# Performance work log

Hardware: AMD Instinct MI355X
Metric: run time of the kernel (lower is better)

## Reference

```python
import jax, jax.numpy as jnp
import numpy as np

N, E, IN, H, O, ED = 20000, 100000, 167, 4, 256, 10
HID = H * O  # 1024
BN_EPS = 1e-5


def _bn(x, g, b):
    # BatchNorm1d in training mode: batch statistics over nodes
    mu = x.mean(0)
    var = x.var(0)
    return (x - mu) * jax.lax.rsqrt(var + BN_EPS) * g + b


def _gat(x, src, dst, ef, Wg, We, attn, at, cb, heads, out):
    # modified_GAT: multi-head attention with edge features + time scalar
    n = x.shape[0]
    h = (x @ Wg).reshape(n, heads, out)                 # [N,H,O]
    e = (ef[:, 1:] @ We).reshape(-1, heads, out)        # [E,H,O] edge-feature proj
    t = ef[:, 0]                                        # [E] time feature
    # node-level attention scores (avoids materializing [E,H,O] twice)
    s_src = jnp.einsum('nhd,hd->nh', h, attn[0])
    s_dst = jnp.einsum('nhd,hd->nh', h, attn[1])
    s_e = jnp.einsum('ehd,hd->eh', e, attn[2])
    logits = jax.nn.leaky_relu(s_src[src] + s_dst[dst] + s_e + t[:, None] * at, 0.2)  # [E,H]
    # attention normalization: softmax over incoming edges of each dst node
    m = jax.ops.segment_max(logits, dst, num_segments=n)
    m = jnp.where(jnp.isfinite(m), m, 0.0)
    p = jnp.exp(logits - m[dst])
    denom = jax.ops.segment_sum(p, dst, num_segments=n)
    w = p / (denom[dst] + 1e-16)                        # [E,H]
    msg = w[:, :, None] * (h[src] + e)                  # [E,H,O]
    agg = jax.ops.segment_sum(msg, dst, num_segments=n) # [N,H,O]
    return agg.reshape(n, heads * out) + cb


def setup_inputs() -> dict:
    key = jax.random.key(0)
    ks = iter(jax.random.split(key, 64))

    def nrm(shape, s):
        return jax.random.normal(next(ks), shape, dtype=jnp.float32) * np.float32(s)

    d = {}
    d['x'] = jax.random.normal(next(ks), (N, IN), dtype=jnp.float32)
    d['edge_index'] = jax.random.randint(next(ks), (2, E), 0, N)
    d['edge_attr'] = jax.random.uniform(next(ks), (E, ED + 2), dtype=jnp.float32)
    conv_dims = [(IN, H, O), (HID, H, O), (HID, 1, 2)]
    for i, (fin, hh, oo) in enumerate(conv_dims, 1):
        d[f'Wg{i}'] = nrm((fin, hh * oo), 1.0 / np.sqrt(fin))
        d[f'We{i}'] = nrm((ED, hh * oo), 1.0 / np.sqrt(ED))
        d[f'attn{i}'] = nrm((3, hh, oo), 0.1)
        d[f'at{i}'] = nrm((hh,), 0.1)
        d[f'cb{i}'] = jnp.zeros((hh * oo,), jnp.float32)
    lin_dims = [(IN, HID), (HID, HID), (HID, 2)]
    bn_dims = [IN, HID, HID]
    for i, (fin, fo) in enumerate(lin_dims, 1):
        d[f'lw{i}'] = nrm((fin, fo), 1.0 / np.sqrt(fin))
        d[f'lb{i}'] = jnp.zeros((fo,), jnp.float32)
        d[f'g{i}'] = jnp.ones((bn_dims[i - 1],), jnp.float32)
        d[f'b{i}'] = jnp.zeros((bn_dims[i - 1],), jnp.float32)
    return d


def reference(x, edge_index, edge_attr,
              Wg1, We1, attn1, at1, cb1, lw1, lb1, g1, b1,
              Wg2, We2, attn2, at2, cb2, lw2, lb2, g2, b2,
              Wg3, We3, attn3, at3, cb3, lw3, lb3, g3, b3):
    src, dst = edge_index[0], edge_index[1]
    ef = edge_attr[:, :-1]  # drop edge class column
    h = _bn(x, g1, b1)
    h = jax.nn.relu(h @ lw1 + lb1 + _gat(h, src, dst, ef, Wg1, We1, attn1, at1, cb1, H, O))
    h = _bn(h, g2, b2)
    h = jax.nn.relu(h @ lw2 + lb2 + _gat(h, src, dst, ef, Wg2, We2, attn2, at2, cb2, H, O))
    h = _bn(h, g3, b3)
    h = jax.nn.relu(h @ lw3 + lb3 + _gat(h, src, dst, ef, Wg3, We3, attn3, at3, cb3, 1, 2))
    return h
```

## Files before the change

### kernel.cpp

```cpp
#include <hip/hip_runtime.h>
#include <math.h>

#define NN 20000
#define EE 100000
#define FIN 167
#define KP1 256
#define HID 1024
#define OO 256
#define NB 8

typedef unsigned short u16;
typedef short bf16x8 __attribute__((ext_vector_type(8)));
typedef short s16x4  __attribute__((ext_vector_type(4)));
typedef float f32x4  __attribute__((ext_vector_type(4)));

__device__ __forceinline__ float bf(u16 u){ return __uint_as_float(((unsigned)u)<<16); }
__device__ __forceinline__ u16 fb(float v){
  unsigned u = __float_as_uint(v);
  return (u16)((u + 0x7FFFu + ((u>>16)&1u)) >> 16);
}
__device__ __forceinline__ float ldv(const float* p, long i){ return p[i]; }
__device__ __forceinline__ float ldv(const u16*   p, long i){ return bf(p[i]); }

__global__ void k_count(const int* __restrict__ ei, int* __restrict__ counts){
  int e = blockIdx.x*256 + threadIdx.x;
  if (e < EE) atomicAdd(&counts[ei[EE+e]], 1);
}

__global__ __launch_bounds__(256) void k_scanA(const int* __restrict__ counts,
                                               int* __restrict__ iptr, int* __restrict__ bsum){
  __shared__ int sd[256];
  int b = blockIdx.x, tid = threadIdx.x;
  int i = b*256 + tid;
  int v = (i<NN)? counts[i] : 0;
  sd[tid]=v; __syncthreads();
  for (int off=1; off<256; off<<=1){
    int t = (tid>=off)? sd[tid-off] : 0;
    __syncthreads();
    sd[tid] += t;
    __syncthreads();
  }
  if (i<NN) iptr[i] = sd[tid]-v;
  if (tid==255) bsum[b]=sd[255];
}
__global__ __launch_bounds__(128) void k_scanB(const int* __restrict__ bsum,
                                               int* __restrict__ boff, int* __restrict__ iptrN,
                                               int nb){
  __shared__ int sd[128];
  int tid=threadIdx.x;
  int v=(tid<nb)? bsum[tid]:0;
  sd[tid]=v; __syncthreads();
  for (int off=1; off<128; off<<=1){
    int t=(tid>=off)?sd[tid-off]:0;
    __syncthreads();
    sd[tid]+=t;
    __syncthreads();
  }
  if (tid<nb) boff[tid]=sd[tid]-v;
  if (tid==127) *iptrN = sd[127];
}
__global__ void k_scanC(const int* __restrict__ boff, int* __restrict__ iptr){
  int i = blockIdx.x*256+threadIdx.x;
  if (i<NN) iptr[i] += boff[blockIdx.x];
}

__global__ void k_fill(const int* __restrict__ ei, const int* __restrict__ iptr,
                       int* __restrict__ cursor, int* __restrict__ eid){
  int e = blockIdx.x*256 + threadIdx.x;
  if (e < EE){
    int d = ei[EE+e];
    int pos = atomicAdd(&cursor[d],1);
    eid[iptr[d]+pos] = e;
  }
}

template<typename T>
__global__ void k_bnstats(const T* __restrict__ X, float* __restrict__ sums, int F){
  int f = blockIdx.y*256 + threadIdx.x;
  if (f >= F) return;
  int r0 = blockIdx.x*100, r1 = r0+100;
  float s=0.f, s2=0.f;
  for (int r=r0;r<r1;r++){ float v = ldv(X,(long)r*F+f); s += v; s2 += v*v; }
  atomicAdd(&sums[f], s);
  atomicAdd(&sums[F+f], s2);
}

__global__ __launch_bounds__(256) void k_bnstats8(const u16* __restrict__ X, float* __restrict__ part){
  int tid = threadIdx.x;
  int f8 = (tid & 127)*8;
  int r0 = blockIdx.x*79, r1 = min(NN, r0+79);
  float s[8]={0,0,0,0,0,0,0,0}, s2[8]={0,0,0,0,0,0,0,0};
  for (int r=r0 + (tid>>7); r<r1; r+=2){
    bf16x8 v = *(const bf16x8*)(X + (long)r*HID + f8);
    #pragma unroll
    for (int j=0;j<8;j++){ float x=bf((u16)v[j]); s[j]+=x; s2[j]+=x*x; }
  }
  __shared__ float red[256][8];
  float* pb = part + (long)blockIdx.x*2048;
  #pragma unroll
  for (int j=0;j<8;j++) red[tid][j]=s[j];
  __syncthreads();
  if (tid<128){
    #pragma unroll
    for (int j=0;j<8;j++) pb[f8+j] = red[tid][j]+red[tid+128][j];
  }
  __syncthreads();
  #pragma unroll
  for (int j=0;j<8;j++) red[tid][j]=s2[j];
  __syncthreads();
  if (tid<128){
    #pragma unroll
    for (int j=0;j<8;j++) pb[1024+f8+j] = red[tid][j]+red[tid+128][j];
  }
}

__global__ __launch_bounds__(256) void k_pred(const float* __restrict__ part, float* __restrict__ sums){
  int idx = blockIdx.x*256 + threadIdx.x;
  float s = 0.f;
  #pragma unroll 8
  for (int b=0;b<256;b++) s += part[(long)b*2048 + idx];
  sums[idx] = s;
}

__global__ void k_bnfin(const float* __restrict__ sums, const float* __restrict__ g,
                        const float* __restrict__ b, float* __restrict__ scale,
                        float* __restrict__ shift, int F){
  int f = blockIdx.x*256 + threadIdx.x;
  if (f >= F) return;
  float mu  = sums[f]   * (1.f/NN);
  float var = sums[F+f] * (1.f/NN) - mu*mu;
  float sc  = rsqrtf(var + 1e-5f) * g[f];
  scale[f] = sc;
  shift[f] = b[f] - mu*sc;
}

__global__ __launch_bounds__(256) void k_foldT(const float* __restrict__ Wg, const float* __restrict__ Wl,
                        const float* __restrict__ scale,
                        u16* __restrict__ Wt, int K, int Kp){
  __shared__ float t[32][33];
  int k0 = blockIdx.x*32, c0 = blockIdx.y*32;
  int tx = threadIdx.x & 31, ty = threadIdx.x >> 5;
  bool second = (c0 >= HID);
  const float* W = second ? Wl : Wg;
  int cc0 = second ? c0 - HID : c0;
  #pragma unroll
  for (int i=0;i<4;i++){
    int k = k0 + ty + i*8;
    t[ty+i*8][tx] = (k < K) ? W[(long)k*HID + cc0 + tx] * scale[k] : 0.f;
  }
  __syncthreads();
  #pragma unroll
  for (int i=0;i<4;i++){
    int c = c0 + ty + i*8;
    Wt[(long)c*Kp + k0 + tx] = fb(t[tx][ty+i*8]);
  }
}

__global__ void k_cinit(const float* __restrict__ lb, float* __restrict__ cst){
  int c = blockIdx.x*256 + threadIdx.x;
  if (c < 2*HID) cst[c] = (c >= HID) ? lb[c-HID] : 0.f;
}

__global__ __launch_bounds__(256) void k_const(const float* __restrict__ Wg, const float* __restrict__ Wl,
                        const float* __restrict__ shift, float* __restrict__ cst, int K){
  int tx = threadIdx.x & 63, ty = threadIdx.x >> 6;
  int c = blockIdx.x*64 + tx;
  bool second = c >= HID;
  const float* W = second ? Wl : Wg;
  int cc = second ? c-HID : c;
  int k0 = blockIdx.y*128;
  int k1 = min(K, k0+128);
  float s = 0.f;
  for (int k=k0+ty; k<k1; k+=4) s += shift[k]*W[(long)k*HID+cc];
  __shared__ float red[256];
  red[threadIdx.x] = s;
  __syncthreads();
  if (ty == 0){
    float tot = red[tx] + red[tx+64] + red[tx+128] + red[tx+192];
    atomicAdd(&cst[c], tot);
  }
}

__global__ void k_cast(const float* __restrict__ x, u16* __restrict__ xb){
  long idx = (long)blockIdx.x*256 + threadIdx.x;
  if (idx >= (long)NN*KP1) return;
  int n = (int)(idx / KP1), k = (int)(idx % KP1);
  xb[idx] = (k<FIN)? fb(x[(long)n*FIN+k]) : (u16)0;
}

__global__ void k_we16(const float* __restrict__ We, u16* __restrict__ We16){
  int i = blockIdx.x*256 + threadIdx.x;
  if (i < 10*HID) We16[i] = fb(We[i]);
}

#define MF(a_,b_,c_) __builtin_amdgcn_mfma_f32_16x16x32_bf16(a_,b_,c_,0,0,0)
#define FENCE asm volatile("" ::: "memory")
#define BAR do { FENCE; __builtin_amdgcn_s_barrier(); FENCE; } while(0)

__global__ __launch_bounds__(512,2) void k_gemm(const u16* __restrict__ A, int K,
                     const u16* __restrict__ Wt, const float* __restrict__ cst,
                     u16* __restrict__ Chg, u16* __restrict__ Clin){
  __shared__ u16 lds[2][24576];
  int b = blockIdx.x;
  int wg = (b & 7)*158 + (b >> 3);
  int row0 = (wg >> 4)*256, col0 = (wg & 15)*128;
  int tid = threadIdx.x;
  int wave = tid >> 6, lane = tid & 63, quad = lane >> 4, lo = lane & 15;
  int wm = wave >> 1, wn = wave & 1;
  const u16* Apt[2];
  #pragma unroll
  for (int i=0;i<2;i++){
    int s = i*512 + tid, srow = s>>2;
    int gr = row0 + srow; if (gr >= NN) gr = NN-1;
    Apt[i] = A + (long)gr*K + (((s&3)^(srow&3))*8);
  }
  int brow = tid>>2;
  const u16* Bpt = Wt + (long)(col0 + brow)*K + ((((tid&3)^(brow&3)))*8);
  const char* ldsc = (const char*)&lds[0][0];
  int axor = lo & 3;
  int aoff = (wm*64 + lo)*64 + ((quad^axor)*16);
  int boff = 32768 + (wn*64 + lo)*64 + ((quad^axor)*16);
  int NT = K >> 6;
  f32x4 acc[4][4] = {};
  {
    u16* d = (u16*)&lds[0][0];
    __builtin_amdgcn_global_load_lds(Apt[0],      d +          tid*8, 16, 0, 0);
    __builtin_amdgcn_global_load_lds(Apt[1],      d +  4096 +  tid*8, 16, 0, 0);
    __builtin_amdgcn_global_load_lds(Bpt,         d + 16384 +  tid*8, 16, 0, 0);
    __builtin_amdgcn_global_load_lds(Apt[0] + 32, d +  8192 +  tid*8, 16, 0, 0);
    __builtin_amdgcn_global_load_lds(Apt[1] + 32, d + 12288 +  tid*8, 16, 0, 0);
    __builtin_amdgcn_global_load_lds(Bpt    + 32, d + 20480 +  tid*8, 16, 0, 0);
    asm volatile("s_waitcnt vmcnt(3)" ::: "memory");
    BAR;
  }
  for (int t=0; t<NT; t++){
    const char* Lb = ldsc + (t&1)*49152;
    u16* Sb = (u16*)&lds[0][0] + ((t&1)^1)*24576;
    int k0n = (t+1) << 6;
    int nx = (t+1 < NT);
    bf16x8 af[4], bfr[4];
    #pragma unroll
    for (int i=0;i<4;i++) af[i]  = *(const bf16x8*)(Lb + aoff + i*1024);
    #pragma unroll
    for (int n=0;n<4;n++) bfr[n] = *(const bf16x8*)(Lb + boff + n*1024);
    if (nx){
      __builtin_amdgcn_global_load_lds(Apt[0] + k0n, Sb +          tid*8, 16, 0, 0);
      __builtin_amdgcn_global_load_lds(Apt[1] + k0n, Sb +  4096 +  tid*8, 16, 0, 0);
      __builtin_amdgcn_global_load_lds(Bpt    + k0n, Sb + 16384 +  tid*8, 16, 0, 0);
    }
    #pragma unroll
    for (int i=0;i<4;i++)
      #pragma unroll
      for (int n=0;n<4;n++)
        acc[i][n] = MF(af[i], bfr[n], acc[i][n]);
    if (nx) asm volatile("s_waitcnt vmcnt(3)" ::: "memory");
    else    asm volatile("s_waitcnt vmcnt(0)" ::: "memory");
    BAR;
    #pragma unroll
    for (int i=0;i<4;i++) af[i]  = *(const bf16x8*)(Lb + 16384 + aoff + i*1024);
    #pragma unroll
    for (int n=0;n<4;n++) bfr[n] = *(const bf16x8*)(Lb +  8192 + boff + n*1024);
    if (nx){
      __builtin_amdgcn_global_load_lds(Apt[0] + k0n + 32, Sb +  8192 +  tid*8, 16, 0, 0);
      __builtin_amdgcn_global_load_lds(Apt[1] + k0n + 32, Sb + 12288 +  tid*8, 16, 0, 0);
      __builtin_amdgcn_global_load_lds(Bpt    + k0n + 32, Sb + 20480 +  tid*8, 16, 0, 0);
    }
    #pragma unroll
    for (int i=0;i<4;i++)
      #pragma unroll
      for (int n=0;n<4;n++)
        acc[i][n] = MF(af[i], bfr[n], acc[i][n]);
    if (nx) asm volatile("s_waitcnt vmcnt(3)" ::: "memory");
    BAR;
  }
  #pragma unroll
  for (int i=0;i<4;i++){
    #pragma unroll
    for (int n=0;n<4;n++){
      int col = col0 + wn*64 + n*16 + lo;
      float cs = cst[col];
      #pragma unroll
      for (int r=0;r<4;r++){
        int row = row0 + wm*64 + i*16 + quad*4 + r;
        if (row < NN){
          u16 o = fb(acc[i][n][r] + cs);
          if (col < HID) Chg[(long)row*HID + col] = o;
          else           Clin[(long)row*HID + col - HID] = o;
        }
      }
    }
  }
}
#undef MF
#undef BAR
#undef FENCE

__global__ __launch_bounds__(256) void k_sdot(const u16* __restrict__ hg, const float* __restrict__ attn,
                       float* __restrict__ ssrc, float* __restrict__ sdst){
  int unit = blockIdx.x*4 + (threadIdx.x >> 6);
  if (unit >= NN*4) return;
  int lane = threadIdx.x & 63;
  int n = unit >> 2, h = unit & 3;
  const u16* hp = hg + (long)n*HID + h*OO + lane*4;
  s16x4 v = *(const s16x4*)hp;
  float4 x0 = *(const float4*)(attn + h*OO + lane*4);
  float4 x1 = *(const float4*)(attn + HID + h*OO + lane*4);
  float f0 = bf((u16)v.x), f1 = bf((u16)v.y), f2 = bf((u16)v.z), f3 = bf((u16)v.w);
  float ss = f0*x0.x + f1*x0.y + f2*x0.z + f3*x0.w;
  float sd = f0*x1.x + f1*x1.y + f2*x1.z + f3*x1.w;
  #pragma unroll
  for (int off=32; off>0; off>>=1){
    ss += __shfl_down(ss, off);
    sd += __shfl_down(sd, off);
  }
  if (lane==0){ ssrc[unit]=ss; sdst[unit]=sd; }
}

__global__ void k_q(const float* __restrict__ We, const float* __restrict__ attn,
                    float* __restrict__ q){
  int t = threadIdx.x;
  if (t >= 40) return;
  int k = t >> 2, h = t & 3;
  float s = 0.f;
  for (int d=0; d<OO; d++) s += We[(long)k*HID + h*OO + d] * attn[2*HID + h*OO + d];
  q[k*4+h] = s;
}

__global__ void k_logits(const int* __restrict__ ei, const float* __restrict__ ea,
                         const float* __restrict__ q, const float* __restrict__ at,
                         const float* __restrict__ ssrc, const float* __restrict__ sdst,
                         float* __restrict__ L){
  int e = blockIdx.x*256 + threadIdx.x;
  if (e >= EE) return;
  int s = ei[e], dd = ei[EE+e];
  float4 a0 = *(const float4*)(ea + (long)e*12);
  float4 a1 = *(const float4*)(ea + (long)e*12 + 4);
  float4 a2 = *(const float4*)(ea + (long)e*12 + 8);
  float t = a0.x;
  float cc[10] = {a0.y,a0.z,a0.w, a1.x,a1.y,a1.z,a1.w, a2.x,a2.y,a2.z};
  float4 ss = *(const float4*)(ssrc + (long)s*4);
  float4 sd = *(const float4*)(sdst + (long)dd*4);
  float sv[4] = {ss.x+sd.x, ss.y+sd.y, ss.z+sd.z, ss.w+sd.w};
  float4 out;
  #pragma unroll
  for (int h=0;h<4;h++){
    float se = 0.f;
    #pragma unroll
    for (int k=0;k<10;k++) se += cc[k]*q[k*4+h];
    float v = sv[h] + se + t*at[h];
    ((float*)&out)[h] = (v>0.f)? v : 0.2f*v;
  }
  *(float4*)(L + (long)e*4) = out;
}

__global__ void k_mden(const int* __restrict__ iptr, const int* __restrict__ eid,
                       const float* __restrict__ ea, float* __restrict__ L,
                       float* __restrict__ cw){
  int n = blockIdx.x*256 + threadIdx.x;
  if (n >= NN) return;
  int b = iptr[n], e1 = iptr[n+1];
  float m0=-INFINITY, m1=-INFINITY, m2=-INFINITY, m3=-INFINITY;
  for (int i=b;i<e1;i++){
    float4 l = *(const float4*)(L + (long)eid[i]*4);
    m0=fmaxf(m0,l.x); m1=fmaxf(m1,l.y); m2=fmaxf(m2,l.z); m3=fmaxf(m3,l.w);
  }
  if (b==e1){ m0=m1=m2=m3=0.f; }
  float s0=0.f,s1=0.f,s2=0.f,s3=0.f;
  for (int i=b;i<e1;i++){
    float4 l = *(const float4*)(L + (long)eid[i]*4);
    s0+=expf(l.x-m0); s1+=expf(l.y-m1); s2+=expf(l.z-m2); s3+=expf(l.w-m3);
  }
  float d0=1.f/(s0+1e-16f), d1=1.f/(s1+1e-16f), d2=1.f/(s2+1e-16f), d3=1.f/(s3+1e-16f);
  float c[4][10] = {};
  for (int i=b;i<e1;i++){
    int e = eid[i];
    float4 l = *(const float4*)(L + (long)e*4);
    float4 w = { expf(l.x-m0)*d0, expf(l.y-m1)*d1, expf(l.z-m2)*d2, expf(l.w-m3)*d3 };
    *(float4*)(L + (long)e*4) = w;
    float4 a0 = *(const float4*)(ea + (long)e*12);
    float4 a1 = *(const float4*)(ea + (long)e*12 + 4);
    float4 a2 = *(const float4*)(ea + (long)e*12 + 8);
    float cc[10] = {a0.y,a0.z,a0.w, a1.x,a1.y,a1.z,a1.w, a2.x,a2.y,a2.z};
    #pragma unroll
    for (int k=0;k<10;k++){
      c[0][k] += w.x*cc[k]; c[1][k] += w.y*cc[k];
      c[2][k] += w.z*cc[k]; c[3][k] += w.w*cc[k];
    }
  }
  float* cp = cw + (long)n*40;
  #pragma unroll
  for (int h=0;h<4;h++)
    #pragma unroll
    for (int k=0;k<10;k++) cp[h*10+k] = c[h][k];
}

__global__ __launch_bounds__(256) void k_gath(
    const u16* __restrict__ hg, const int* __restrict__ ei,
    const int* __restrict__ iptr, const int* __restrict__ eid,
    const float* __restrict__ L,
    const float* __restrict__ cw,
    const u16* __restrict__ We16, const float* __restrict__ cb,
    u16* __restrict__ lio)
{
  __shared__ u16  sWe[10*HID];
  __shared__ float scb[HID];
  int tid = threadIdx.x;
  for (int i=tid;i<10*HID;i+=256) sWe[i] = We16[i];
  for (int i=tid;i<HID;i+=256) scb[i] = cb[i];
  __syncthreads();
  int h = tid >> 6;
  int f0 = tid*4;
  int d0 = blockIdx.x*NB, dend = min(NN, d0+NB);
  for (int d=d0; d<dend; d++){
    s16x4 a0 = *(const s16x4*)(lio + (long)d*HID + f0);
    float acc0=bf((u16)a0.x), acc1=bf((u16)a0.y), acc2=bf((u16)a0.z), acc3=bf((u16)a0.w);
    int b0 = iptr[d], en = iptr[d+1];
    float wN = 0.f; s16x4 vN = {};
    if (b0 < en){
      int e = eid[b0], s_ = ei[e];
      wN = L[(long)e*4 + h];
      vN = *(const s16x4*)(hg + (long)s_*HID + f0);
    }
    for (int i=b0;i<en;i++){
      float w = wN; s16x4 v = vN;
      if (i+1 < en){
        int e2 = eid[i+1], s2 = ei[e2];
        wN = L[(long)e2*4 + h];
        vN = *(const s16x4*)(hg + (long)s2*HID + f0);
      }
      acc0 += w*bf((u16)v.x); acc1 += w*bf((u16)v.y);
      acc2 += w*bf((u16)v.z); acc3 += w*bf((u16)v.w);
    }
    const float* cp = cw + (long)d*40 + h*10;
    float ew0=0.f, ew1=0.f, ew2=0.f, ew3=0.f;
    #pragma unroll
    for (int k=0;k<10;k++){
      float c = cp[k];
      s16x4 wv = *(const s16x4*)(sWe + k*HID + f0);
      ew0 += c*bf((u16)wv.x); ew1 += c*bf((u16)wv.y);
      ew2 += c*bf((u16)wv.z); ew3 += c*bf((u16)wv.w);
    }
    acc0 += ew0; acc1 += ew1; acc2 += ew2; acc3 += ew3;
    u16 o[4];
    o[0] = fb(fmaxf(acc0 + scb[f0  ], 0.f));
    o[1] = fb(fmaxf(acc1 + scb[f0+1], 0.f));
    o[2] = fb(fmaxf(acc2 + scb[f0+2], 0.f));
    o[3] = fb(fmaxf(acc3 + scb[f0+3], 0.f));
    *(s16x4*)(lio + (long)d*HID + f0) = *(const s16x4*)o;
  }
}

__global__ void k_c4init(const float* __restrict__ lb, float* __restrict__ c4){
  if (threadIdx.x==0 && blockIdx.x==0){ c4[0]=0.f; c4[1]=0.f; c4[2]=lb[0]; c4[3]=lb[1]; }
}

__global__ __launch_bounds__(256) void k_fold3(const float* __restrict__ Wg, const float* __restrict__ lw,
                        const float* __restrict__ scale, const float* __restrict__ shift,
                        float* __restrict__ W4, float* __restrict__ c4){
  int k = blockIdx.x*256 + threadIdx.x;
  float sc = scale[k], sh = shift[k];
  float w0=Wg[k*2], w1=Wg[k*2+1], l0=lw[k*2], l1=lw[k*2+1];
  float4 o = {w0*sc, w1*sc, l0*sc, l1*sc};
  *(float4*)(W4 + (long)k*4) = o;
  __shared__ float red[256][4];
  int tid = threadIdx.x;
  red[tid][0]=sh*w0; red[tid][1]=sh*w1; red[tid][2]=sh*l0; red[tid][3]=sh*l1;
  __syncthreads();
  for (int o2=128;o2>0;o2>>=1){
    if (tid<o2){
      #pragma unroll
      for (int j=0;j<4;j++) red[tid][j]+=red[tid+o2][j];
    }
    __syncthreads();
  }
  if (tid==0){
    #pragma unroll
    for (int j=0;j<4;j++) atomicAdd(&c4[j], red[0][j]);
  }
}

__global__ __launch_bounds__(256) void k_n3(const u16* __restrict__ in,
    const float* __restrict__ W4, const float* __restrict__ c4,
    const float* __restrict__ attn,
    float* __restrict__ hg3, float* __restrict__ lin3,
    float* __restrict__ ssrc, float* __restrict__ sdst)
{
  __shared__ float sW[HID*4];
  __shared__ float sx[4][HID];
  int tid = threadIdx.x;
  int n0 = blockIdx.x*4;
  for (int i=tid; i<HID; i+=256) *(float4*)&sW[i*4] = *(const float4*)(W4 + (long)i*4);
  for (int idx=tid; idx<512; idx+=256){
    int rr = idx>>7, ch = idx&127;
    bf16x8 v = *(const bf16x8*)(in + (long)(n0+rr)*HID + ch*8);
    #pragma unroll
    for (int j=0;j<8;j++) sx[rr][ch*8+j] = bf((u16)v[j]);
  }
  __syncthreads();
  int w = tid>>6, lane = tid&63;
  float p0=0.f,p1=0.f,p2=0.f,p3=0.f;
  #pragma unroll
  for (int g=0; g<16; g++){
    int k = g*64 + lane;
    float x = sx[w][k];
    float4 wv = *(const float4*)&sW[k*4];
    p0 += x*wv.x; p1 += x*wv.y; p2 += x*wv.z; p3 += x*wv.w;
  }
  #pragma unroll
  for (int off=32; off>0; off>>=1){
    p0 += __shfl_down(p0, off);
    p1 += __shfl_down(p1, off);
    p2 += __shfl_down(p2, off);
    p3 += __shfl_down(p3, off);
  }
  if (lane==0){
    int n = n0 + w;
    float r0=p0+c4[0], r1=p1+c4[1], r2=p2+c4[2], r3=p3+c4[3];
    hg3[n*2]=r0; hg3[n*2+1]=r1;
    lin3[n*2]=r2; lin3[n*2+1]=r3;
    ssrc[n]=r0*attn[0]+r1*attn[1];
    sdst[n]=r0*attn[2]+r1*attn[3];
  }
}

__global__ void k_logits3(const int* __restrict__ ei, const float* __restrict__ ea,
                          const float* __restrict__ We, const float* __restrict__ attn,
                          const float* __restrict__ at, const float* __restrict__ ssrc,
                          const float* __restrict__ sdst, float* __restrict__ L){
  int e = blockIdx.x*256 + threadIdx.x;
  if (e >= EE) return;
  int s = ei[e], d = ei[EE+e];
  float e0=0.f, e1=0.f;
  #pragma unroll
  for (int k=0;k<10;k++){
    float c = ea[e*12+1+k];
    e0 += c*We[k*2]; e1 += c*We[k*2+1];
  }
  float se = e0*attn[4] + e1*attn[5];
  float v = ssrc[s] + sdst[d] + se + ea[e*12]*at[0];
  L[e] = (v>0.f)? v : 0.2f*v;
}

__global__ void k_mden3(const int* __restrict__ iptr, const int* __restrict__ eid,
                        const float* __restrict__ ea, float* __restrict__ L,
                        float* __restrict__ cw){
  int n = blockIdx.x*256 + threadIdx.x;
  if (n >= NN) return;
  int b = iptr[n], e1 = iptr[n+1];
  float mx = -INFINITY;
  for (int i=b;i<e1;i++) mx = fmaxf(mx, L[eid[i]]);
  if (b == e1) mx = 0.f;
  float s = 0.f;
  for (int i=b;i<e1;i++) s += expf(L[eid[i]] - mx);
  float dv = 1.f/(s+1e-16f);
  float c[10] = {0.f,0.f,0.f,0.f,0.f,0.f,0.f,0.f,0.f,0.f};
  for (int i=b;i<e1;i++){
    int e = eid[i];
    float w = expf(L[e]-mx)*dv;
    L[e] = w;
    #pragma unroll
    for (int k=0;k<10;k++) c[k] += w*ea[e*12+1+k];
  }
  float* cp = cw + (long)n*10;
  #pragma unroll
  for (int k=0;k<10;k++) cp[k] = c[k];
}

__global__ void k_gather3(const int* __restrict__ ei,
                          const int* __restrict__ iptr, const int* __restrict__ eid,
                          const float* __restrict__ L,
                          const float* __restrict__ cw,
                          const float* __restrict__ hg3,
                          const float* __restrict__ We, const float* __restrict__ lin3,
                          const float* __restrict__ cb, float* __restrict__ out){
  int n = blockIdx.x*256 + threadIdx.x;
  if (n >= NN) return;
  int b = iptr[n], en = iptr[n+1];
  const float* cp = cw + (long)n*10;
  float e0f=0.f, e1f=0.f;
  #pragma unroll
  for (int k=0;k<10;k++){ e0f += cp[k]*We[k*2]; e1f += cp[k]*We[k*2+1]; }
  float a0=0.f, a1=0.f;
  for (int i=b;i<en;i++){
    int e = eid[i], s_ = ei[e];
    float w = L[e];
    a0 += w*hg3[s_*2];
    a1 += w*hg3[s_*2+1];
  }
  out[n*2]   = fmaxf(lin3[n*2]  +a0+e0f+cb[0], 0.f);
  out[n*2+1] = fmaxf(lin3[n*2+1]+a1+e1f+cb[1], 0.f);
}

extern "C" void kernel_launch(void* const* d_in, const int* in_sizes, int n_in,
                              void* d_out, int out_size, void* d_ws, size_t ws_size,
                              hipStream_t stream){
  const int* ei = (const int*)d_in[1];

  long long sz[64];
  {
    const long long* s64 = (const long long*)(const void*)in_sizes;
    bool is64 = (n_in >= 2) && (in_sizes[0] == 3340000) && (in_sizes[1] == 0)
                && (s64[1] == 200000);
    for (int i=0;i<n_in && i<64;i++) sz[i] = is64 ? s64[i] : (long long)in_sizes[i];
  }

  int IWg[3], IWe[3], IAttn[3], IAt[3], ICb[3], ILw[3], ILb[3], IG[3], IB[3];
  if (n_in > 8 && sz[8] == (long long)HID*HID){
    for (int l=0;l<3;l++){
      IWg[l]=3+l*5; IWe[l]=4+l*5; IAttn[l]=5+l*5; IAt[l]=6+l*5; ICb[l]=7+l*5;
      ILw[l]=18+l*4; ILb[l]=19+l*4; IG[l]=20+l*4; IB[l]=21+l*4;
    }
  } else {
    int idx=3;
    for (int l=0;l<3;l++){
      IWg[l]=idx++; IWe[l]=idx++; IAttn[l]=idx++; IAt[l]=idx++; ICb[l]=idx++;
      ILw[l]=idx++; ILb[l]=idx++; IG[l]=idx++; IB[l]=idx++;
    }
  }
  #define FP(i) ((const float*)d_in[(i)])

  char* ws = (char*)d_ws;
  size_t off = 0;
  auto alloc = [&](size_t bytes)->void*{ void* p = ws + off; off += (bytes + 255) & ~(size_t)255; return p; };
  auto G = [](long n){ return (int)((n+255)/256); };

  u16*   buf0 = (u16*)  alloc((size_t)NN*HID*2);
  u16*   bufA = (u16*)  alloc((size_t)NN*HID*2);
  u16*   bufB = (u16*)  alloc((size_t)NN*HID*2);
  u16*   xbf  = (u16*)  alloc((size_t)NN*KP1*2);
  u16*   Wt   = (u16*)  alloc((size_t)2*HID*HID*2);
  u16*   We16 = (u16*)  alloc((size_t)10*HID*2);
  float* cst  = (float*)alloc(2*HID*4);
  float* L    = (float*)alloc((size_t)EE*4*4);
  float* ssrc = (float*)alloc((size_t)NN*4*4);
  float* sdst = (float*)alloc((size_t)NN*4*4);
  int*   iptr = (int*)  alloc((size_t)(NN+4)*4);
  int*   cnts = (int*)  alloc((size_t)NN*4);
  int*   eid  = (int*)  alloc((size_t)EE*4);
  int*   bsum = (int*)  alloc(256*4);
  int*   boff = (int*)  alloc(256*4);
  float* stats= (float*)alloc(2*HID*4);
  float* scale= (float*)alloc(HID*4);
  float* shift= (float*)alloc(HID*4);
  float* qbuf = (float*)alloc(64*4);
  float* hg3  = (float*)alloc((size_t)NN*2*4);
  float* lin3 = (float*)alloc((size_t)NN*2*4);
  float* cw   = (float*)alloc((size_t)NN*40*4);
  float* W4   = (float*)alloc((size_t)HID*4*4);
  float* c4   = (float*)alloc(4*4);
  float* part = (float*)alloc((size_t)256*2048*4);

  int nsb = G(NN);
  hipMemsetAsync(cnts, 0, NN*sizeof(int), stream);
  k_count<<<G(EE),256,0,stream>>>(ei, cnts);
  k_scanA<<<nsb,256,0,stream>>>(cnts, iptr, bsum);
  k_scanB<<<1,128,0,stream>>>(bsum, boff, iptr+NN, nsb);
  k_scanC<<<nsb,256,0,stream>>>(boff, iptr);
  hipMemsetAsync(cnts, 0, NN*sizeof(int), stream);
  k_fill<<<G(EE),256,0,stream>>>(ei, iptr, cnts, eid);

  int gg = 1264;
  int gsd = (NN*4+3)/4;

  {
    hipMemsetAsync(stats, 0, 2*FIN*sizeof(float), stream);
    dim3 bg(200, 1);
    k_bnstats<float><<<bg,256,0,stream>>>(FP(0), stats, FIN);
    k_bnfin<<<1,256,0,stream>>>(stats, FP(IG[0]), FP(IB[0]), scale, shift, FIN);
    k_cast<<<G((long)NN*KP1),256,0,stream>>>(FP(0), xbf);
    dim3 ft(KP1/32, 64);
    k_foldT<<<ft,256,0,stream>>>(FP(IWg[0]), FP(ILw[0]), scale, Wt, FIN, KP1);
    k_cinit<<<8,256,0,stream>>>(FP(ILb[0]), cst);
    dim3 cg(32, (FIN+127)/128);
    k_const<<<cg,256,0,stream>>>(FP(IWg[0]), FP(ILw[0]), shift, cst, FIN);
    k_we16<<<40,256,0,stream>>>(FP(IWe[0]), We16);
    k_gemm<<<gg,512,0,stream>>>(xbf, KP1, Wt, cst, buf0, bufA);
    k_sdot<<<gsd,256,0,stream>>>(buf0, FP(IAttn[0]), ssrc, sdst);
    k_q<<<1,64,0,stream>>>(FP(IWe[0]), FP(IAttn[0]), qbuf);
    k_logits<<<G(EE),256,0,stream>>>(ei, FP(2), qbuf, FP(IAt[0]), ssrc, sdst, L);
    k_mden<<<G(NN),256,0,stream>>>(iptr, eid, FP(2), L, cw);
    k_gath<<<(NN+NB-1)/NB,256,0,stream>>>(buf0, ei, iptr, eid, L, cw,
                                          We16, FP(ICb[0]), bufA);
  }
  {
    k_bnstats8<<<256,256,0,stream>>>(bufA, part);
    k_pred<<<8,256,0,stream>>>(part, stats);
    k_bnfin<<<4,256,0,stream>>>(stats, FP(IG[1]), FP(IB[1]), scale, shift, HID);
    dim3 ft(HID/32, 64);
    k_foldT<<<ft,256,0,stream>>>(FP(IWg[1]), FP(ILw[1]), scale, Wt, HID, HID);
    k_cinit<<<8,256,0,stream>>>(FP(ILb[1]), cst);
    dim3 cg(32, HID/128);
    k_const<<<cg,256,0,stream>>>(FP(IWg[1]), FP(ILw[1]), shift, cst, HID);
    k_we16<<<40,256,0,stream>>>(FP(IWe[1]), We16);
    k_gemm<<<gg,512,0,stream>>>(bufA, HID, Wt, cst, buf0, bufB);
    k_sdot<<<gsd,256,0,stream>>>(buf0, FP(IAttn[1]), ssrc, sdst);
    k_q<<<1,64,0,stream>>>(FP(IWe[1]), FP(IAttn[1]), qbuf);
    k_logits<<<G(EE),256,0,stream>>>(ei, FP(2), qbuf, FP(IAt[1]), ssrc, sdst, L);
    k_mden<<<G(NN),256,0,stream>>>(iptr, eid, FP(2), L, cw);
    k_gath<<<(NN+NB-1)/NB,256,0,stream>>>(buf0, ei, iptr, eid, L, cw,
                                          We16, FP(ICb[1]), bufB);
  }

  k_bnstats8<<<256,256,0,stream>>>(bufB, part);
  k_pred<<<8,256,0,stream>>>(part, stats);
  k_bnfin<<<4,256,0,stream>>>(stats, FP(IG[2]), FP(IB[2]), scale, shift, HID);
  k_c4init<<<1,64,0,stream>>>(FP(ILb[2]), c4);
  k_fold3<<<HID/256,256,0,stream>>>(FP(IWg[2]), FP(ILw[2]), scale, shift, W4, c4);
  k_n3<<<NN/4,256,0,stream>>>(bufB, W4, c4, FP(IAttn[2]), hg3, lin3, ssrc, sdst);
  k_logits3<<<G(EE),256,0,stream>>>(ei, FP(2), FP(IWe[2]), FP(IAttn[2]), FP(IAt[2]), ssrc, sdst, L);
  k_mden3<<<G(NN),256,0,stream>>>(iptr, eid, FP(2), L, cw);
  k_gather3<<<G(NN),256,0,stream>>>(ei, iptr, eid, L, cw, hg3,
                                    FP(IWe[2]), lin3, FP(ICb[2]), (float*)d_out);
}
```

Before: 815.3 us.

## Use triple-buffered LDS ring with prefetch distance two in GEMM

```diff
diff --git a/kernel.cpp b/kernel.cpp
--- a/kernel.cpp
+++ b/kernel.cpp
@@ -200,7 +200,7 @@
 __global__ __launch_bounds__(512,2) void k_gemm(const u16* __restrict__ A, int K,
                      const u16* __restrict__ Wt, const float* __restrict__ cst,
                      u16* __restrict__ Chg, u16* __restrict__ Clin){
-  __shared__ u16 lds[2][24576];
+  __shared__ u16 lds[3][12288];
   int b = blockIdx.x;
   int wg = (b & 7)*158 + (b >> 3);
   int row0 = (wg >> 4)*256, col0 = (wg & 15)*128;
@@ -219,59 +219,49 @@
   const char* ldsc = (const char*)&lds[0][0];
   int axor = lo & 3;
   int aoff = (wm*64 + lo)*64 + ((quad^axor)*16);
-  int boff = 32768 + (wn*64 + lo)*64 + ((quad^axor)*16);
-  int NT = K >> 6;
+  int boff = 16384 + (wn*64 + lo)*64 + ((quad^axor)*16);
+  int NT = K >> 5;
   f32x4 acc[4][4] = {};
   {
-    u16* d = (u16*)&lds[0][0];
-    __builtin_amdgcn_global_load_lds(Apt[0],      d +          tid*8, 16, 0, 0);
-    __builtin_amdgcn_global_load_lds(Apt[1],      d +  4096 +  tid*8, 16, 0, 0);
-    __builtin_amdgcn_global_load_lds(Bpt,         d + 16384 +  tid*8, 16, 0, 0);
-    __builtin_amdgcn_global_load_lds(Apt[0] + 32, d +  8192 +  tid*8, 16, 0, 0);
-    __builtin_amdgcn_global_load_lds(Apt[1] + 32, d + 12288 +  tid*8, 16, 0, 0);
-    __builtin_amdgcn_global_load_lds(Bpt    + 32, d + 20480 +  tid*8, 16, 0, 0);
+    u16* d0 = (u16*)&lds[0][0];
+    u16* d1 = (u16*)&lds[1][0];
+    __builtin_amdgcn_global_load_lds(Apt[0],      d0 +         tid*8, 16, 0, 0);
+    __builtin_amdgcn_global_load_lds(Apt[1],      d0 + 4096 +  tid*8, 16, 0, 0);
+    __builtin_amdgcn_global_load_lds(Bpt,         d0 + 8192 +  tid*8, 16, 0, 0);
+    __builtin_amdgcn_global_load_lds(Apt[0] + 32, d1 +         tid*8, 16, 0, 0);
+    __builtin_amdgcn_global_load_lds(Apt[1] + 32, d1 + 4096 +  tid*8, 16, 0, 0);
+    __builtin_amdgcn_global_load_lds(Bpt    + 32, d1 + 8192 +  tid*8, 16, 0, 0);
     asm volatile("s_waitcnt vmcnt(3)" ::: "memory");
     BAR;
   }
+  int cb = 0;
   for (int t=0; t<NT; t++){
-    const char* Lb = ldsc + (t&1)*49152;
-    u16* Sb = (u16*)&lds[0][0] + ((t&1)^1)*24576;
-    int k0n = (t+1) << 6;
-    int nx = (t+1 < NT);
+    const char* Lb = ldsc + cb*24576;
     bf16x8 af[4], bfr[4];
     #pragma unroll
     for (int i=0;i<4;i++) af[i]  = *(const bf16x8*)(Lb + aoff + i*1024);
     #pragma unroll
     for (int n=0;n<4;n++) bfr[n] = *(const bf16x8*)(Lb + boff + n*1024);
-    if (nx){
-      __builtin_amdgcn_global_load_lds(Apt[0] + k0n, Sb +          tid*8, 16, 0, 0);
-      __builtin_amdgcn_global_load_lds(Apt[1] + k0n, Sb +  4096 +  tid*8, 16, 0, 0);
-      __builtin_amdgcn_global_load_lds(Bpt    + k0n, Sb + 16384 +  tid*8, 16, 0, 0);
+    int nx2 = (t+2 < NT);
+    if (nx2){
+      int sb = cb+2; if (sb>=3) sb-=3;
+      u16* Sd = (u16*)&lds[0][0] + sb*12288;
+      int ko = (t+2) << 5;
+      __builtin_amdgcn_global_load_lds(Apt[0] + ko, Sd +         tid*8, 16, 0, 0);
+      __builtin_amdgcn_global_load_lds(Apt[1] + ko, Sd + 4096 +  tid*8, 16, 0, 0);
+      __builtin_amdgcn_global_load_lds(Bpt    + ko, Sd + 8192 +  tid*8, 16, 0, 0);
     }
     #pragma unroll
     for (int i=0;i<4;i++)
       #pragma unroll
       for (int n=0;n<4;n++)
         acc[i][n] = MF(af[i], bfr[n], acc[i][n]);
-    if (nx) asm volatile("s_waitcnt vmcnt(3)" ::: "memory");
-    else    asm volatile("s_waitcnt vmcnt(0)" ::: "memory");
-    BAR;
-    #pragma unroll
-    for (int i=0;i<4;i++) af[i]  = *(const bf16x8*)(Lb + 16384 + aoff + i*1024);
-    #pragma unroll
-    for (int n=0;n<4;n++) bfr[n] = *(const bf16x8*)(Lb +  8192 + boff + n*1024);
-    if (nx){
-      __builtin_amdgcn_global_load_lds(Apt[0] + k0n + 32, Sb +  8192 +  tid*8, 16, 0, 0);
-      __builtin_amdgcn_global_load_lds(Apt[1] + k0n + 32, Sb + 12288 +  tid*8, 16, 0, 0);
-      __builtin_amdgcn_global_load_lds(Bpt    + k0n + 32, Sb + 20480 +  tid*8, 16, 0, 0);
-    }
-    #pragma unroll
-    for (int i=0;i<4;i++)
-      #pragma unroll
-      for (int n=0;n<4;n++)
-        acc[i][n] = MF(af[i], bfr[n], acc[i][n]);
-    if (nx) asm volatile("s_waitcnt vmcnt(3)" ::: "memory");
-    BAR;
+    if (t+1 < NT){
+      if (nx2) asm volatile("s_waitcnt vmcnt(3)" ::: "memory");
+      else     asm volatile("s_waitcnt vmcnt(0)" ::: "memory");
+      BAR;
+    }
+    cb++; if (cb>=3) cb=0;
   }
   #pragma unroll
   for (int i=0;i<4;i++){
```

Measured after the change: 765.4 us. -6.1%, faster.
